# Kernel tuning notes

Hardware: AMD Instinct MI355X
Metric: run time of the kernel (lower is better)

The kernel has to match this reference:

```python
import jax, jax.numpy as jnp
import numpy as np

B, G, C, Hmlp, R = 4, 2048, 384, 1536, 96
NH = 6          # attention heads
V = 6           # number of 2D views (len(out_transform_2d))
NC = 1024       # number of clusters for segment_csr
GX = GY = 32    # grid shape per view
SCALE_FACTOR = 0.5  # args.scale_factor
COEF_PRO = 0.5      # args.coef_pro
EPS_LN = 1e-5
EPS_BN = 1e-5


def _forward(x, center1, norm1_g, norm1_b, qkv_w, proj_w, proj_b, norm2_g, norm2_b,
             fc1_w, fc1_b, fc2_w, fc2_b, ada1_w, ada1_b, ada2_w, ada2_b,
             bn3_g, bn3_b, bn3_m, bn3_v, bn2_g, bn2_b, bn2_m, bn2_v,
             norm3_g, norm3_b, a1_qkv_w, a1_proj_w, a1_proj_b,
             mask, idx_ptr, sorted_cluster_indices, cluster, flat_grid_index,
             grid_shape_x, grid_shape_y):
    B_, G1, C_ = x.shape
    hd = C_ // NH

    def ln(t, g, b):
        mu = t.mean(-1, keepdims=True)
        var = ((t - mu) ** 2).mean(-1, keepdims=True)
        return (t - mu) * jax.lax.rsqrt(var + EPS_LN) * g + b

    def bn_gelu(t, g, b, m, v):  # BatchNorm1d (eval) + GELU
        t = (t - m) * jax.lax.rsqrt(v + EPS_BN) * g + b
        return jax.nn.gelu(t, approximate=False)

    # ---- multi-head self-attention sublayer ----
    h = ln(x, norm1_g, norm1_b)
    qkv = (h @ qkv_w).reshape(B_, G1, 3, NH, hd).transpose(2, 0, 3, 1, 4)
    q, k, v = qkv[0], qkv[1], qkv[2]
    attn = jax.nn.softmax(jnp.einsum('bhqd,bhkd->bhqk', q, k) * hd ** -0.5, axis=-1)
    o = jnp.einsum('bhqk,bhkd->bhqd', attn, v).transpose(0, 2, 1, 3).reshape(B_, G1, C_)
    x = x + o @ proj_w + proj_b

    # ---- MLP + adapter sublayer ----
    h2 = ln(x, norm2_g, norm2_b)
    ffn = jax.nn.gelu(h2 @ fc1_w + fc1_b, approximate=False) @ fc2_w + fc2_b
    a = ffn @ ada1_w + ada1_b
    a = a * jax.nn.sigmoid(1.702 * a)      # QuickGELU
    ada = a @ ada2_w + ada2_b
    x = x + ffn + SCALE_FACTOR * ada

    cls_x = x[:, :1]
    pts = x[:, 1:]
    Gp = G1 - 1
    N = B_ * Gp

    # ---- 3D branch: segment_csr max/mean over clusters, gather back ----
    feat = pts.reshape(N, C_)
    fs = feat[sorted_cluster_indices]
    seg = cluster[sorted_cluster_indices]          # sorted segment ids (CSR order)
    nc = idx_ptr.shape[0] - 1
    cnt = jax.ops.segment_sum(jnp.ones((N,), feat.dtype), seg, nc)
    fsum = jax.ops.segment_sum(fs, seg, nc)
    fmax = jax.ops.segment_max(fs, seg, nc)
    fmax = jnp.where(cnt[:, None] > 0, fmax, 0.0)
    fmean = fsum / jnp.maximum(cnt, 1.0)[:, None]
    x3d = bn_gelu(fmax + fmean, bn3_g, bn3_b, bn3_m, bn3_v)[cluster].reshape(pts.shape)

    # ---- per-view 2D branch: masked attn + scatter_max/mean over grid cells ----
    dim_size = center1.shape[0] * grid_shape_x * grid_shape_y
    nviews = center1.shape[1]
    views = []
    for i in range(nviews):
        fx = pts.reshape(N, C_)
        h3 = ln(fx, norm3_g[i], norm3_b[i]).reshape(B_, Gp, C_)
        qkv1 = (h3 @ a1_qkv_w[i]).reshape(B_, Gp, 3, C_).transpose(2, 0, 1, 3)
        q1, k1, v1 = qkv1[0], qkv1[1], qkv1[2]
        s = jnp.einsum('bqd,bkd->bqk', q1, k1) * C_ ** -0.5
        s = jnp.where(mask[i][None], s, jnp.finfo(s.dtype).min)
        o1 = jnp.einsum('bqk,bkd->bqd', jax.nn.softmax(s, axis=-1), v1) @ a1_proj_w[i] + a1_proj_b[i]
        fx = o1.reshape(N, C_) + fx
        gi = flat_grid_index[i]
        gc = jax.ops.segment_sum(jnp.ones((N,), fx.dtype), gi, dim_size)
        gs = jax.ops.segment_sum(fx, gi, dim_size)
        gm = jax.ops.segment_max(fx, gi, dim_size)
        gm = jnp.where(gc[:, None] > 0, gm, 0.0)
        cell = bn_gelu(gs / jnp.maximum(gc, 1.0)[:, None] + gm,
                       bn2_g[i], bn2_b[i], bn2_m[i], bn2_v[i])
        views.append(cell[gi].reshape(pts.shape))

    # ---- cosine-similarity weighted fusion across views ----
    x_sup = jnp.stack(views, 0)                     # [V,B,G,C]
    dot = jnp.sum(x_sup * x3d[None], -1)
    nrm = jnp.linalg.norm(x_sup, axis=-1) * jnp.linalg.norm(x3d, axis=-1)[None]
    sims = (dot / jnp.maximum(nrm, 1e-8) + 1.0) / 2.0
    sims = sims / sims.sum(0, keepdims=True)
    x_sup_w = jnp.sum(x_sup * sims[..., None], 0)
    pts = pts + COEF_PRO * x_sup_w
    return jnp.concatenate([cls_x, pts], axis=1)


def setup_inputs() -> dict:
    rng = np.random.default_rng(0)
    key = jax.random.key(0)
    N = B * G
    # consistent cluster structure: every cluster non-empty
    cluster = np.concatenate([np.arange(NC), rng.integers(0, NC, N - NC)]).astype(np.int32)
    rng.shuffle(cluster)
    sorted_idx = np.argsort(cluster, kind='stable').astype(np.int32)
    counts = np.bincount(cluster, minlength=NC)
    idx_ptr = np.concatenate([[0], np.cumsum(counts)]).astype(np.int32)
    flat_grid_index = rng.integers(0, B * GX * GY, (V, N)).astype(np.int32)
    mask = (rng.random((V, G, G)) < 0.25) | np.eye(G, dtype=bool)[None]
    ks = jax.random.split(key, 16)
    f32 = jnp.float32
    def w(k, shape, s=0.02):
        return jax.random.normal(k, shape, f32) * s
    return {
        'x': jax.random.normal(ks[0], (B, G + 1, C), f32),
        'center1': jax.random.normal(ks[1], (B, V, G, 3), f32),
        'norm1_g': jnp.ones((C,), f32), 'norm1_b': jnp.zeros((C,), f32),
        'qkv_w': w(ks[2], (C, 3 * C)), 'proj_w': w(ks[3], (C, C)), 'proj_b': jnp.zeros((C,), f32),
        'norm2_g': jnp.ones((C,), f32), 'norm2_b': jnp.zeros((C,), f32),
        'fc1_w': w(ks[4], (C, Hmlp)), 'fc1_b': jnp.zeros((Hmlp,), f32),
        'fc2_w': w(ks[5], (Hmlp, C)), 'fc2_b': jnp.zeros((C,), f32),
        'ada1_w': w(ks[6], (C, R)), 'ada1_b': jnp.zeros((R,), f32),
        'ada2_w': w(ks[7], (R, C)), 'ada2_b': jnp.zeros((C,), f32),
        'bn3_g': jnp.ones((C,), f32), 'bn3_b': jnp.zeros((C,), f32),
        'bn3_m': w(ks[8], (C,), 0.1), 'bn3_v': jnp.ones((C,), f32) + jax.random.uniform(ks[9], (C,), f32) * 0.5,
        'bn2_g': jnp.ones((V, C), f32), 'bn2_b': jnp.zeros((V, C), f32),
        'bn2_m': w(ks[10], (V, C), 0.1), 'bn2_v': jnp.ones((V, C), f32) + jax.random.uniform(ks[11], (V, C), f32) * 0.5,
        'norm3_g': jnp.ones((V, C), f32), 'norm3_b': jnp.zeros((V, C), f32),
        'a1_qkv_w': w(ks[12], (V, C, 3 * C)), 'a1_proj_w': w(ks[13], (V, C, C)), 'a1_proj_b': jnp.zeros((V, C), f32),
        'mask': jnp.asarray(mask),
        'idx_ptr': jnp.asarray(idx_ptr),
        'sorted_cluster_indices': jnp.asarray(sorted_idx),
        'cluster': jnp.asarray(cluster),
        'flat_grid_index': jnp.asarray(flat_grid_index),
        'grid_shape_x': GX,
        'grid_shape_y': GY,
    }


def reference(x, center1, norm1_g, norm1_b, qkv_w, proj_w, proj_b, norm2_g, norm2_b,
              fc1_w, fc1_b, fc2_w, fc2_b, ada1_w, ada1_b, ada2_w, ada2_b,
              bn3_g, bn3_b, bn3_m, bn3_v, bn2_g, bn2_b, bn2_m, bn2_v,
              norm3_g, norm3_b, a1_qkv_w, a1_proj_w, a1_proj_b,
              mask, idx_ptr, sorted_cluster_indices, cluster, flat_grid_index,
              grid_shape_x, grid_shape_y):
    return _forward(x, center1, norm1_g, norm1_b, qkv_w, proj_w, proj_b, norm2_g, norm2_b,
                    fc1_w, fc1_b, fc2_w, fc2_b, ada1_w, ada1_b, ada2_w, ada2_b,
                    bn3_g, bn3_b, bn3_m, bn3_v, bn2_g, bn2_b, bn2_m, bn2_v,
                    norm3_g, norm3_b, a1_qkv_w, a1_proj_w, a1_proj_b,
                    mask, idx_ptr, sorted_cluster_indices, cluster, flat_grid_index,
                    grid_shape_x, grid_shape_y)
```

## Files before the change

### kernel.cpp

```cpp
#include <hip/hip_runtime.h>
#include <math.h>

typedef short bf16x8 __attribute__((ext_vector_type(8)));
typedef float f32x4 __attribute__((ext_vector_type(4)));

#define GLL16(g, l) \
  __builtin_amdgcn_global_load_lds((__attribute__((address_space(1))) const unsigned int*)(g), \
                                   (__attribute__((address_space(3))) unsigned int*)(l), 16, 0, 0)

__device__ __forceinline__ float wsum(float v){
  #pragma unroll
  for (int o=32;o;o>>=1) v += __shfl_xor(v,o);
  return v;
}
__device__ __forceinline__ float geluf(float x){
  return 0.5f*x*(1.0f+erff(x*0.7071067811865475f));
}
__device__ __forceinline__ short fbf(float f){
  unsigned u = __float_as_uint(f);
  unsigned r = (u + 0x7fffu + ((u>>16)&1u)) >> 16;
  return (short)r;
}
__device__ __forceinline__ float bff(short s){
  return __uint_as_float(((unsigned)(unsigned short)s)<<16);
}
__device__ __forceinline__ unsigned fkey(float f){
  unsigned b=__float_as_uint(f);
  return (b&0x80000000u)? ~b : (b|0x80000000u);
}
__device__ __forceinline__ float fdec(unsigned k){
  unsigned b=(k&0x80000000u)? (k&0x7fffffffu) : ~k;
  return __uint_as_float(b);
}

__global__ void mask_bits_kernel(const void* __restrict__ m, unsigned long long* __restrict__ mb,
                                 long long nOut, int mode){
  long long i = (long long)blockIdx.x*256 + threadIdx.x;
  if (i>=nOut) return;
  unsigned long long bits = 0;
  if (mode){
    const unsigned long long* p = (const unsigned long long*)((const unsigned char*)m + i*64);
    #pragma unroll
    for (int k=0;k<8;k++){
      unsigned long long v = p[k];
      #pragma unroll
      for (int b=0;b<8;b++)
        bits |= (unsigned long long)(((v>>(b*8))&0xffull)!=0) << (k*8+b);
    }
  } else {
    const int4* p = (const int4*)((const int*)m + i*64);
    #pragma unroll
    for (int k=0;k<16;k++){
      int4 v = p[k];
      bits |= (unsigned long long)(v.x!=0) << (k*4+0);
      bits |= (unsigned long long)(v.y!=0) << (k*4+1);
      bits |= (unsigned long long)(v.z!=0) << (k*4+2);
      bits |= (unsigned long long)(v.w!=0) << (k*4+3);
    }
  }
  mb[i] = bits;
}

__device__ __forceinline__ float epi(float v, const float* bias, int col, int act){
  if (bias) v += bias[col];
  if (act==1) v = geluf(v);
  else if (act==2) v = v*(1.f/(1.f+__expf(-1.702f*v)));
  return v;
}

#define XBM 128
#define XBN 128
#define XBK 32
__global__ __launch_bounds__(256)
void gemm_bf16_big(const short* __restrict__ A, int lda, long long sA,
                   const short* __restrict__ B, int ldb, long long sB,
                   const float* __restrict__ bias, long long sBias,
                   const float* __restrict__ res, int ldr, long long sR,
                   void* __restrict__ out, int ldo, long long sO, int outbf16,
                   int M, int N, int K, int act, int KS)
{
  __shared__ short As[XBM*XBK];
  __shared__ short Bs[XBN*XBK];
  int zz = blockIdx.z;
  int z = zz / KS, ks = zz - z*KS;
  A += (long long)z*sA; B += (long long)z*sB;
  if (res) res += (long long)z*sR;
  if (bias) bias += (long long)z*sBias;
  float* outF = (float*)out + (long long)z*sO;
  short* outH = (short*)out + (long long)z*sO;

  int tid = threadIdx.x;
  int rowBase = blockIdx.y*XBM;
  int colBase = blockIdx.x*XBN;

  int Kc = ((K + KS*XBK - 1)/(KS*XBK))*XBK;
  int kbeg = ks*Kc;
  int kend = min(K, kbeg+Kc);
  if (kbeg >= kend) return;

  int w = tid>>6;
  int lane = tid&63;
  int lm = lane&15, quad = lane>>4;
  int waveM = w>>1, waveN = w&1;

  int arow0 = min(rowBase + w*32 + lm,      M-1);
  int arow1 = min(rowBase + w*32 + 16 + lm, M-1);
  int brow0 = min(colBase + w*32 + lm,      N-1);
  int brow1 = min(colBase + w*32 + 16 + lm, N-1);
  const short* Ag0 = A + (long long)arow0*lda + quad*8;
  const short* Ag1 = A + (long long)arow1*lda + quad*8;
  const short* Bg0 = B + (long long)brow0*ldb + quad*8;
  const short* Bg1 = B + (long long)brow1*ldb + quad*8;
  short* Al0 = &As[(w*2+0)*512];
  short* Al1 = &As[(w*2+1)*512];
  short* Bl0 = &Bs[(w*2+0)*512];
  short* Bl1 = &Bs[(w*2+1)*512];

  f32x4 acc[4][4] = {};

  for (int k0=kbeg; k0<kend; k0+=XBK){
    GLL16(Ag0 + k0, Al0);
    GLL16(Ag1 + k0, Al1);
    GLL16(Bg0 + k0, Bl0);
    GLL16(Bg1 + k0, Bl1);
    __syncthreads();
    bf16x8 af[4], bfr[4];
    #pragma unroll
    for (int tm=0;tm<4;tm++) af[tm]  = *(bf16x8*)&As[(waveM*4+tm)*512 + quad*128 + lm*8];
    #pragma unroll
    for (int tn=0;tn<4;tn++) bfr[tn] = *(bf16x8*)&Bs[(waveN*4+tn)*512 + quad*128 + lm*8];
    #pragma unroll
    for (int tm=0;tm<4;tm++)
      #pragma unroll
      for (int tn=0;tn<4;tn++)
        acc[tm][tn] = __builtin_amdgcn_mfma_f32_16x16x32_bf16(af[tm], bfr[tn], acc[tm][tn], 0,0,0);
    __syncthreads();
  }

  #pragma unroll
  for (int tm=0;tm<4;tm++){
    #pragma unroll
    for (int tn=0;tn<4;tn++){
      int col = colBase + waveN*64 + tn*16 + lm;
      if (col>=N) continue;
      #pragma unroll
      for (int reg=0;reg<4;reg++){
        int row = rowBase + waveM*64 + tm*16 + quad*4 + reg;
        if (row>=M) continue;
        float v = acc[tm][tn][reg];
        if (KS>1){ atomicAdd(&outF[(long long)row*ldo+col], v); continue; }
        v = epi(v, bias, col, act);
        if (res) v += res[(long long)row*ldr+col];
        if (outbf16) outH[(long long)row*ldo+col] = fbf(v);
        else         outF[(long long)row*ldo+col] = v;
      }
    }
  }
}

__global__ __launch_bounds__(256)
void gemm_bf16_s(const short* __restrict__ A, int lda, long long sA,
                 const short* __restrict__ B, int ldb, long long sB,
                 const float* __restrict__ bias, long long sBias,
                 const float* __restrict__ res, int ldr, long long sR,
                 void* __restrict__ out, int ldo, long long sO, int outbf16,
                 int M, int N, int K, int act, short* __restrict__ out2)
{
  __shared__ short As[64*32];
  __shared__ short Bs[64*32];
  int z = blockIdx.z;
  A += (long long)z*sA; B += (long long)z*sB;
  if (res) res += (long long)z*sR;
  if (bias) bias += (long long)z*sBias;
  float* outF = (float*)out + (long long)z*sO;
  short* outH = (short*)out + (long long)z*sO;

  int tid = threadIdx.x;
  int rowBase = blockIdx.y*64;
  int colBase = blockIdx.x*64;

  int w = tid>>6;
  int lane = tid&63;
  int lm = lane&15, quad = lane>>4;
  int wm = w>>1, wn = w&1;

  int arow = min(rowBase + w*16 + lm, M-1);
  int brow = min(colBase + w*16 + lm, N-1);
  const short* Ag = A + (long long)arow*lda + quad*8;
  const short* Bg = B + (long long)brow*ldb + quad*8;
  short* Al = &As[w*512];
  short* Bl = &Bs[w*512];

  f32x4 acc[2][2] = {};

  for (int k0=0; k0<K; k0+=32){
    GLL16(Ag + k0, Al);
    GLL16(Bg + k0, Bl);
    __syncthreads();
    bf16x8 af[2], bfr[2];
    #pragma unroll
    for (int tm=0;tm<2;tm++) af[tm]  = *(bf16x8*)&As[(wm*2+tm)*512 + quad*128 + lm*8];
    #pragma unroll
    for (int tn=0;tn<2;tn++) bfr[tn] = *(bf16x8*)&Bs[(wn*2+tn)*512 + quad*128 + lm*8];
    #pragma unroll
    for (int tm=0;tm<2;tm++)
      #pragma unroll
      for (int tn=0;tn<2;tn++)
        acc[tm][tn] = __builtin_amdgcn_mfma_f32_16x16x32_bf16(af[tm], bfr[tn], acc[tm][tn], 0,0,0);
    __syncthreads();
  }

  #pragma unroll
  for (int tm=0;tm<2;tm++){
    #pragma unroll
    for (int tn=0;tn<2;tn++){
      int col = colBase + wn*32 + tn*16 + lm;
      if (col>=N) continue;
      #pragma unroll
      for (int reg=0;reg<4;reg++){
        int row = rowBase + wm*32 + tm*16 + quad*4 + reg;
        if (row>=M) continue;
        float v = epi(acc[tm][tn][reg], bias, col, act);
        if (res) v += res[(long long)row*ldr+col];
        if (outbf16==2){
          int bb = row>>11;
          outH[((long long)bb*384 + col)*2176 + (row&2047)] = fbf(v);
        }
        else if (outbf16) outH[(long long)row*ldo+col] = fbf(v);
        else {
          outF[(long long)row*ldo+col] = v;
          if (out2) out2[(long long)row*ldo+col] = fbf(v);
        }
      }
    }
  }
}

__global__ __launch_bounds__(256,2)
void flash_view(const short* __restrict__ QK6, const short* __restrict__ Vt6,
                const unsigned long long* __restrict__ maskbits, short* __restrict__ O6)
{
  __shared__ char lds[58112];
  const float scale = 0.05103103630798288f;
  int id = blockIdx.x;
  int xcd = id & 7;
  int j = id >> 3;
  int vb = xcd*3 + (j>>5);
  int qt = j & 31;
  int v = vb >> 2, b = vb & 3;
  int tid=threadIdx.x, w=tid>>6, lane=tid&63, lm=lane&15, quad=lane>>4;

  const short* Qp = QK6 + ((long long)v*8192 + b*2048 + qt*64)*768;
  const short* Kp = QK6 + ((long long)v*8192 + b*2048)*768 + 384;
  const short* Vp = Vt6 + (long long)(v*4+b)*384*2048;
  const unsigned long long* Mb = maskbits + (long long)v*2048*32 + (long long)qt*64*32;
  short* Op = O6 + ((long long)v*8192 + b*2048 + qt*64)*384;

  short* P = (short*)(lds + 49152);
  float* alphaL = (float*)(lds + 57856);

  bf16x8 af[12];
  #pragma unroll
  for (int c=0;c<12;c++)
    af[c] = *(const bf16x8*)(Qp + (long long)(w*16+lm)*768 + c*32 + quad*8);

  float m_i[4], l_i[4];
  #pragma unroll
  for (int r=0;r<4;r++){ m_i[r]=-3.0e38f; l_i[r]=0.f; }
  f32x4 Oacc[4][6] = {};

  for (int kt=0; kt<32; kt++){
    #pragma unroll
    for (int c=0;c<12;c++)
      GLL16(Kp + (long long)(kt*64 + w*16 + lm)*768 + c*32 + quad*8, (short*)(lds + w*12288 + c*1024));
    __syncthreads();
    unsigned long long mb[4];
    #pragma unroll
    for (int r=0;r<4;r++)
      mb[r] = Mb[(long long)(w*16+quad*4+r)*32 + kt];
    f32x4 S[4];
    #pragma unroll
    for (int i=0;i<4;i++) S[i] = (f32x4){0.f,0.f,0.f,0.f};
    __builtin_amdgcn_s_setprio(1);
    #pragma unroll
    for (int kc=0;kc<12;kc++){
      #pragma unroll
      for (int ct=0;ct<4;ct++){
        bf16x8 bf = *(bf16x8*)(lds + ct*12288 + kc*1024 + quad*256 + lm*16);
        S[ct] = __builtin_amdgcn_mfma_f32_16x16x32_bf16(af[kc], bf, S[ct], 0,0,0);
      }
    }
    __builtin_amdgcn_s_setprio(0);
    #pragma unroll
    for (int r=0;r<4;r++){
      unsigned long long t = mb[r] >> lm;
      S[0][r] = ((unsigned)t      & 1u) ? S[0][r]*scale : -3.0e38f;
      S[1][r] = ((unsigned)(t>>16)& 1u) ? S[1][r]*scale : -3.0e38f;
      S[2][r] = ((unsigned)(t>>32)& 1u) ? S[2][r]*scale : -3.0e38f;
      S[3][r] = ((unsigned)(t>>48)& 1u) ? S[3][r]*scale : -3.0e38f;
    }
    float alpha[4], mnew[4];
    #pragma unroll
    for (int r=0;r<4;r++){
      float rm = S[0][r];
      #pragma unroll
      for (int ct=1;ct<4;ct++) rm = fmaxf(rm, S[ct][r]);
      #pragma unroll
      for (int o=1;o<16;o<<=1) rm = fmaxf(rm, __shfl_xor(rm, o));
      mnew[r] = fmaxf(m_i[r], rm);
      alpha[r] = __expf(m_i[r]-mnew[r]);
      m_i[r] = mnew[r];
    }
    float rs[4] = {0.f,0.f,0.f,0.f};
    #pragma unroll
    for (int ct=0;ct<4;ct++){
      #pragma unroll
      for (int r=0;r<4;r++){
        float sv = S[ct][r];
        float p = (sv > -1.0e37f) ? __expf(sv - mnew[r]) : 0.f;
        rs[r] += p;
        P[(w*16+quad*4+r)*68 + ct*16 + lm] = fbf(p);
      }
    }
    #pragma unroll
    for (int r=0;r<4;r++){
      #pragma unroll
      for (int o=1;o<16;o<<=1) rs[r] += __shfl_xor(rs[r], o);
      l_i[r] = l_i[r]*alpha[r] + rs[r];
    }
    if (lm==0){
      #pragma unroll
      for (int r=0;r<4;r++) alphaL[w*16+quad*4+r] = alpha[r];
    }
    bf16x8 Vreg[6][2];
    #pragma unroll
    for (int jj=0;jj<6;jj++)
      #pragma unroll
      for (int kk=0;kk<2;kk++)
        Vreg[jj][kk] = *(const bf16x8*)(Vp + (long long)((w*6+jj)*16+lm)*2048 + kt*64 + kk*32 + quad*8);
    __syncthreads();
    f32x4 am[4];
    #pragma unroll
    for (int m=0;m<4;m++) am[m] = *(f32x4*)&alphaL[m*16 + quad*4];
    #pragma unroll
    for (int m=0;m<4;m++)
      #pragma unroll
      for (int tn=0;tn<6;tn++)
        Oacc[m][tn] *= am[m];
    __builtin_amdgcn_s_setprio(1);
    #pragma unroll
    for (int kk=0;kk<2;kk++){
      bf16x8 ap[4];
      #pragma unroll
      for (int m=0;m<4;m++) ap[m] = *(bf16x8*)&P[(m*16+lm)*68 + kk*32 + quad*8];
      #pragma unroll
      for (int tn=0;tn<6;tn++){
        #pragma unroll
        for (int m=0;m<4;m++)
          Oacc[m][tn] = __builtin_amdgcn_mfma_f32_16x16x32_bf16(ap[m], Vreg[tn][kk], Oacc[m][tn], 0,0,0);
      }
    }
    __builtin_amdgcn_s_setprio(0);
  }

  __syncthreads();
  if (lm==0){
    #pragma unroll
    for (int r=0;r<4;r++) alphaL[w*16+quad*4+r] = l_i[r];
  }
  __syncthreads();
  f32x4 lv[4];
  #pragma unroll
  for (int m=0;m<4;m++) lv[m] = *(f32x4*)&alphaL[m*16 + quad*4];
  #pragma unroll
  for (int m=0;m<4;m++){
    #pragma unroll
    for (int tn=0;tn<6;tn++){
      #pragma unroll
      for (int reg=0;reg<4;reg++){
        Op[(long long)(m*16+quad*4+reg)*384 + (w*6+tn)*16 + lm] = fbf(Oacc[m][tn][reg] / lv[m][reg]);
      }
    }
  }
}

__global__ __launch_bounds__(256,3)
void flash_inner(const short* __restrict__ QKV, const short* __restrict__ Vt,
                 short* __restrict__ O)
{
  __shared__ char lds[33536];
  int id = blockIdx.x;
  int xcd = id & 7;
  int j = id >> 3;
  int bh = xcd*3 + j/33;
  int qt = j%33;
  int b=bh/6, h=bh-b*6;
  int tid=threadIdx.x, w=tid>>6, lane=tid&63, lm=lane&15, quad=lane>>4;

  const short* Qb = QKV + (long long)b*2049*1152 + h*64;
  const short* Kb = Qb + 384;
  const short* Vtp = Vt + (long long)bh*64*2176;
  short* Op = O + ((long long)b*2049 + qt*64)*384 + h*64;

  short* P = (short*)(lds + 16384);
  float* alphaL = (float*)(lds + 33280);

  int qr = min(qt*64 + w*16 + lm, 2048);
  bf16x8 af[2];
  #pragma unroll
  for (int c=0;c<2;c++)
    af[c] = *(const bf16x8*)(Qb + (long long)qr*1152 + c*32 + quad*8);

  float m_i[4], l_i[4];
  #pragma unroll
  for (int r=0;r<4;r++){ m_i[r]=-3.0e38f; l_i[r]=0.f; }
  f32x4 Oacc[4] = {};

  #pragma unroll
  for (int h2=0;h2<2;h2++){
    int kr0 = min((w*2+h2)*16 + lm, 2048);
    #pragma unroll
    for (int c=0;c<2;c++)
      GLL16(Kb + (long long)kr0*1152 + c*32 + quad*8, (short*)(lds + (w*2+h2)*2048 + c*1024));
  }

  for (int kt=0; kt<17; kt++){
    __syncthreads();
    f32x4 S[8];
    #pragma unroll
    for (int i=0;i<8;i++) S[i] = (f32x4){0.f,0.f,0.f,0.f};
    __builtin_amdgcn_s_setprio(1);
    #pragma unroll
    for (int kc=0;kc<2;kc++){
      #pragma unroll
      for (int ct=0;ct<8;ct++){
        bf16x8 bf = *(bf16x8*)(lds + ct*2048 + kc*1024 + quad*256 + lm*16);
        S[ct] = __builtin_amdgcn_mfma_f32_16x16x32_bf16(af[kc], bf, S[ct], 0,0,0);
      }
    }
    __builtin_amdgcn_s_setprio(0);
    #pragma unroll
    for (int ct=0;ct<8;ct++){
      int scol = kt*128 + ct*16 + lm;
      bool ok = scol <= 2048;
      #pragma unroll
      for (int r=0;r<4;r++) S[ct][r] = ok ? S[ct][r]*0.125f : -3.0e38f;
    }
    float alpha[4], mnew[4];
    #pragma unroll
    for (int r=0;r<4;r++){
      float rm = S[0][r];
      #pragma unroll
      for (int ct=1;ct<8;ct++) rm = fmaxf(rm, S[ct][r]);
      #pragma unroll
      for (int o=1;o<16;o<<=1) rm = fmaxf(rm, __shfl_xor(rm, o));
      mnew[r] = fmaxf(m_i[r], rm);
      alpha[r] = __expf(m_i[r]-mnew[r]);
      m_i[r] = mnew[r];
    }
    float rs[4] = {0.f,0.f,0.f,0.f};
    #pragma unroll
    for (int ct=0;ct<8;ct++){
      #pragma unroll
      for (int r=0;r<4;r++){
        float sv = S[ct][r];
        float p = (sv > -1.0e37f) ? __expf(sv - mnew[r]) : 0.f;
        rs[r] += p;
        P[(w*16+quad*4+r)*132 + ct*16 + lm] = fbf(p);
      }
    }
    #pragma unroll
    for (int r=0;r<4;r++){
      #pragma unroll
      for (int o=1;o<16;o<<=1) rs[r] += __shfl_xor(rs[r], o);
      l_i[r] = l_i[r]*alpha[r] + rs[r];
    }
    if (lm==0){
      #pragma unroll
      for (int r=0;r<4;r++) alphaL[w*16+quad*4+r] = alpha[r];
    }
    bf16x8 Vreg[4];
    #pragma unroll
    for (int kk=0;kk<4;kk++)
      Vreg[kk] = *(const bf16x8*)(Vtp + (long long)(w*16+lm)*2176 + kt*128 + kk*32 + quad*8);
    __syncthreads();
    if (kt < 16){
      #pragma unroll
      for (int h2=0;h2<2;h2++){
        int krn = min((kt+1)*128 + (w*2+h2)*16 + lm, 2048);
        #pragma unroll
        for (int c=0;c<2;c++)
          GLL16(Kb + (long long)krn*1152 + c*32 + quad*8, (short*)(lds + (w*2+h2)*2048 + c*1024));
      }
    }
    f32x4 am[4];
    #pragma unroll
    for (int m=0;m<4;m++) am[m] = *(f32x4*)&alphaL[m*16 + quad*4];
    #pragma unroll
    for (int m=0;m<4;m++) Oacc[m] *= am[m];
    __builtin_amdgcn_s_setprio(1);
    #pragma unroll
    for (int kk=0;kk<4;kk++){
      bf16x8 ap[4];
      #pragma unroll
      for (int m=0;m<4;m++) ap[m] = *(bf16x8*)&P[(m*16+lm)*132 + kk*32 + quad*8];
      #pragma unroll
      for (int m=0;m<4;m++)
        Oacc[m] = __builtin_amdgcn_mfma_f32_16x16x32_bf16(ap[m], Vreg[kk], Oacc[m], 0,0,0);
    }
    __builtin_amdgcn_s_setprio(0);
  }

  __syncthreads();
  if (lm==0){
    #pragma unroll
    for (int r=0;r<4;r++) alphaL[w*16+quad*4+r] = l_i[r];
  }
  __syncthreads();
  f32x4 lv[4];
  #pragma unroll
  for (int m=0;m<4;m++) lv[m] = *(f32x4*)&alphaL[m*16 + quad*4];
  #pragma unroll
  for (int m=0;m<4;m++){
    #pragma unroll
    for (int reg=0;reg<4;reg++){
      int row = qt*64 + m*16 + quad*4 + reg;
      if (row < 2049)
        Op[(long long)(m*16+quad*4+reg)*384 + w*16 + lm] = fbf(Oacc[m][reg] / lv[m][reg]);
    }
  }
}

__global__ __launch_bounds__(128)
void ln_bf16_kernel(const float* __restrict__ in, const float* __restrict__ g,
                    const float* __restrict__ bt, short* __restrict__ out)
{
  long long row = blockIdx.x;
  const float* p = in + row*384;
  int tid = threadIdx.x;
  float v0=p[tid], v1=p[tid+128], v2=p[tid+256];
  float s = v0+v1+v2;
  float ss = v0*v0+v1*v1+v2*v2;
  __shared__ float r1[2], r2[2];
  s = wsum(s); ss = wsum(ss);
  int wid=tid>>6, lane=tid&63;
  if (lane==0){ r1[wid]=s; r2[wid]=ss; }
  __syncthreads();
  float mean=(r1[0]+r1[1])*(1.f/384.f);
  float var =(r2[0]+r2[1])*(1.f/384.f)-mean*mean;
  float rstd=rsqrtf(var+1e-5f);
  short* o = out + row*384;
  o[tid]     = fbf((v0-mean)*rstd*g[tid]+bt[tid]);
  o[tid+128] = fbf((v1-mean)*rstd*g[tid+128]+bt[tid+128]);
  o[tid+256] = fbf((v2-mean)*rstd*g[tid+256]+bt[tid+256]);
}

__global__ __launch_bounds__(128)
void ln6_kernel(const float* __restrict__ in, const float* __restrict__ g6,
                const float* __restrict__ b6, short* __restrict__ out6)
{
  long long row = blockIdx.x;
  const float* p = in + row*384;
  int tid = threadIdx.x;
  float v0=p[tid], v1=p[tid+128], v2=p[tid+256];
  float s = v0+v1+v2;
  float ss = v0*v0+v1*v1+v2*v2;
  __shared__ float r1[2], r2[2];
  s = wsum(s); ss = wsum(ss);
  int wid=tid>>6, lane=tid&63;
  if (lane==0){ r1[wid]=s; r2[wid]=ss; }
  __syncthreads();
  float mean=(r1[0]+r1[1])*(1.f/384.f);
  float var =(r2[0]+r2[1])*(1.f/384.f)-mean*mean;
  float rstd=rsqrtf(var+1e-5f);
  float n0=(v0-mean)*rstd, n1=(v1-mean)*rstd, n2=(v2-mean)*rstd;
  #pragma unroll
  for (int i=0;i<6;i++){
    const float* g = g6 + i*384;
    const float* bt = b6 + i*384;
    short* o = out6 + (long long)i*8192*384 + row*384;
    o[tid]     = fbf(n0*g[tid]+bt[tid]);
    o[tid+128] = fbf(n1*g[tid+128]+bt[tid+128]);
    o[tid+256] = fbf(n2*g[tid+256]+bt[tid+256]);
  }
}

__global__ __launch_bounds__(256)
void tconv_kernel(const float* __restrict__ in, int ldin, long long sIn, long long sIn2, int zmod,
                  int R, int C, short* __restrict__ out, int ldout, long long sOut)
{
  __shared__ float tile[32][33];
  int z = blockIdx.z;
  const float* ip = in + (long long)(z/zmod)*sIn + (long long)(z%zmod)*sIn2;
  short* op = out + (long long)z*sOut;
  int r0 = blockIdx.x*32;
  int c0 = blockIdx.y*32;
  int tx = threadIdx.x&31, ty = threadIdx.x>>5;
  #pragma unroll
  for (int i=0;i<4;i++){
    int r = r0 + ty + i*8, c = c0 + tx;
    tile[ty+i*8][tx] = (r<R && c<C) ? ip[(long long)r*ldin + c] : 0.f;
  }
  __syncthreads();
  #pragma unroll
  for (int i=0;i<4;i++){
    int oc = c0 + ty + i*8;
    int orr = r0 + tx;
    if (oc<C && orr<ldout) op[(long long)oc*ldout + orr] = fbf(tile[tx][ty+i*8]);
  }
}

__global__ __launch_bounds__(256)
void tconv16_kernel(const short* __restrict__ in, int ldin, long long sIn, long long sIn2, int zmod,
                    int R, int C, short* __restrict__ out, int ldout, long long sOut)
{
  __shared__ short tile[32][34];
  int z = blockIdx.z;
  const short* ip = in + (long long)(z/zmod)*sIn + (long long)(z%zmod)*sIn2;
  short* op = out + (long long)z*sOut;
  int r0 = blockIdx.x*32;
  int c0 = blockIdx.y*32;
  int tx = threadIdx.x&31, ty = threadIdx.x>>5;
  #pragma unroll
  for (int i=0;i<4;i++){
    int r = r0 + ty + i*8, c = c0 + tx;
    tile[ty+i*8][tx] = (r<R && c<C) ? ip[(long long)r*ldin + c] : (short)0;
  }
  __syncthreads();
  #pragma unroll
  for (int i=0;i<4;i++){
    int oc = c0 + ty + i*8;
    int orr = r0 + tx;
    if (oc<C && orr<ldout) op[(long long)oc*ldout + orr] = tile[tx][ty+i*8];
  }
}

__global__ void ew_fuse_kernel(const float* __restrict__ x1, const float* __restrict__ ffn,
                               const float* __restrict__ ada,
                               float* __restrict__ ptsb, float* __restrict__ out){
  long long i=(long long)blockIdx.x*256+threadIdx.x;
  if (i >= 8196ll*384) return;
  float v = x1[i] + ffn[i] + 0.5f*ada[i];
  long long row = i/384; int c = (int)(i - row*384);
  long long b = row/2049; long long g = row - b*2049;
  if (g == 0) out[b*2049*384 + c] = v;
  else        ptsb[((b*2048) + (g-1))*384 + c] = v;
}

__global__ __launch_bounds__(128)
void scatter_seg_kernel(const float* __restrict__ feat, const int* __restrict__ seg,
                        float* __restrict__ fsum, unsigned* __restrict__ fmax,
                        float* __restrict__ cnt,
                        long long zFeat, long long zSeg, long long zSum, long long zCnt)
{
  int n = blockIdx.x, z = blockIdx.y;
  feat += (long long)z*zFeat; seg += (long long)z*zSeg;
  fsum += (long long)z*zSum; fmax += (long long)z*zSum; cnt += (long long)z*zCnt;
  int s = seg[n];
  const float* p = feat + (long long)n*384;
  int tid = threadIdx.x;
  #pragma unroll
  for (int k=0;k<3;k++){
    int c = tid + k*128;
    float v = p[c];
    atomicAdd(&fsum[(long long)s*384+c], v);
    atomicMax(&fmax[(long long)s*384+c], fkey(v));
  }
  if (tid==0) atomicAdd(&cnt[s], 1.0f);
}

__global__ __launch_bounds__(128)
void cell_kernel(const float* __restrict__ fsum, const unsigned* __restrict__ fmax,
                 const float* __restrict__ cnt,
                 const float* __restrict__ g, const float* __restrict__ bb,
                 const float* __restrict__ m, const float* __restrict__ v,
                 float* __restrict__ out, long long zSum, long long zCnt, long long zP)
{
  int s = blockIdx.x, z = blockIdx.y;
  fsum += (long long)z*zSum; fmax += (long long)z*zSum; cnt += (long long)z*zCnt;
  g += (long long)z*zP; bb += (long long)z*zP; m += (long long)z*zP; v += (long long)z*zP;
  out += (long long)z*zSum;
  float cn = cnt[s];
  float denom = fmaxf(cn, 1.f);
  int tid = threadIdx.x;
  #pragma unroll
  for (int k=0;k<3;k++){
    int c = tid + k*128;
    float mx = (cn>0.f) ? fdec(fmax[(long long)s*384+c]) : 0.f;
    float t = mx + fsum[(long long)s*384+c]/denom;
    t = (t - m[c])*rsqrtf(v[c]+1e-5f)*g[c] + bb[c];
    out[(long long)s*384+c] = geluf(t);
  }
}

__global__ __launch_bounds__(384)
void combine_kernel(const float* __restrict__ pts, const float* __restrict__ cell3,
                    const int* __restrict__ cluster, const float* __restrict__ cell2,
                    const int* __restrict__ gidx, float* __restrict__ out)
{
  int n = blockIdx.x;
  int tid = threadIdx.x;
  int w = tid>>6, lane = tid&63;
  __shared__ float sdot[6], ssq[6], sn3s;
  __shared__ int soff[6];
  const float* x3 = cell3 + (long long)cluster[n]*384;
  int gi = gidx[(long long)w*8192 + n];
  const float* r = cell2 + ((long long)w*4096 + gi)*384;
  float d=0.f, s2=0.f, q3=0.f;
  #pragma unroll
  for (int k=0;k<6;k++){
    int c = lane + k*64;
    float a = r[c], x = x3[c];
    d += a*x; s2 += a*a; q3 += x*x;
  }
  d = wsum(d); s2 = wsum(s2); q3 = wsum(q3);
  if (lane==0){ sdot[w]=d; ssq[w]=s2; soff[w]=gi; if (w==0) sn3s=q3; }
  __syncthreads();
  float sn3 = sqrtf(sn3s);
  float sims[6]; float ssumv=0.f;
  #pragma unroll
  for (int i=0;i<6;i++){
    float nrm = sqrtf(ssq[i])*sn3;
    float s = (sdot[i]/fmaxf(nrm,1e-8f) + 1.f)*0.5f;
    sims[i]=s; ssumv+=s;
  }
  int c = tid;
  float acc=0.f;
  #pragma unroll
  for (int i=0;i<6;i++){
    const float* rr = cell2 + ((long long)i*4096 + soff[i])*384;
    acc += (sims[i]/ssumv)*rr[c];
  }
  int b = n>>11, gp = n&2047;
  out[((long long)(b*2049 + 1 + gp))*384 + c] = pts[(long long)n*384+c] + 0.5f*acc;
}

static inline void launch_gemm16b(hipStream_t s, const short* A,int lda,long long sA,
  const short* B,int ldb,long long sB, const float* bias, long long sBias,
  const float* res,int ldr,long long sR, void* out,int ldo,long long sO,int outbf16,
  int M,int N,int K,int act,int nz,int KS)
{
  dim3 g((N+XBN-1)/XBN,(M+XBM-1)/XBM,(unsigned)(nz*KS));
  hipLaunchKernelGGL(gemm_bf16_big,g,dim3(256),0,s,
    A,lda,sA,B,ldb,sB,bias,sBias,res,ldr,sR,out,ldo,sO,outbf16,M,N,K,act,KS);
}
static inline void launch_gemm16s(hipStream_t s, const short* A,int lda,long long sA,
  const short* B,int ldb,long long sB, const float* bias, long long sBias,
  const float* res,int ldr,long long sR, void* out,int ldo,long long sO,int outbf16,
  int M,int N,int K,int act,int nz, short* out2=nullptr)
{
  dim3 g((N+63)/64,(M+63)/64,(unsigned)nz);
  hipLaunchKernelGGL(gemm_bf16_s,g,dim3(256),0,s,
    A,lda,sA,B,ldb,sB,bias,sBias,res,ldr,sR,out,ldo,sO,outbf16,M,N,K,act,out2);
}
static inline void launch_tconv(hipStream_t s, const float* in,int ldin,long long sIn,long long sIn2,int zmod,
  int R,int C, short* out,int ldout,long long sOut,int nz)
{
  dim3 g((ldout+31)/32,(C+31)/32,(unsigned)nz);
  hipLaunchKernelGGL(tconv_kernel,g,dim3(256),0,s, in,ldin,sIn,sIn2,zmod,R,C,out,ldout,sOut);
}
static inline void launch_tconv16(hipStream_t s, const short* in,int ldin,long long sIn,long long sIn2,int zmod,
  int R,int C, short* out,int ldout,long long sOut,int nz)
{
  dim3 g((ldout+31)/32,(C+31)/32,(unsigned)nz);
  hipLaunchKernelGGL(tconv16_kernel,g,dim3(256),0,s, in,ldin,sIn,sIn2,zmod,R,C,out,ldout,sOut);
}

extern "C" void kernel_launch(void* const* d_in, const int* in_sizes, int n_in,
                              void* d_out, int out_size, void* d_ws, size_t ws_size,
                              hipStream_t stream)
{
  const float* x       = (const float*)d_in[0];
  const float* norm1_g = (const float*)d_in[2];
  const float* norm1_b = (const float*)d_in[3];
  const float* qkv_w   = (const float*)d_in[4];
  const float* proj_w  = (const float*)d_in[5];
  const float* proj_b  = (const float*)d_in[6];
  const float* norm2_g = (const float*)d_in[7];
  const float* norm2_b = (const float*)d_in[8];
  const float* fc1_w   = (const float*)d_in[9];
  const float* fc1_b   = (const float*)d_in[10];
  const float* fc2_w   = (const float*)d_in[11];
  const float* fc2_b   = (const float*)d_in[12];
  const float* ada1_w  = (const float*)d_in[13];
  const float* ada1_b  = (const float*)d_in[14];
  const float* ada2_w  = (const float*)d_in[15];
  const float* ada2_b  = (const float*)d_in[16];
  const float* bn3_g   = (const float*)d_in[17];
  const float* bn3_b   = (const float*)d_in[18];
  const float* bn3_m   = (const float*)d_in[19];
  const float* bn3_v   = (const float*)d_in[20];
  const float* bn2_g   = (const float*)d_in[21];
  const float* bn2_b   = (const float*)d_in[22];
  const float* bn2_m   = (const float*)d_in[23];
  const float* bn2_v   = (const float*)d_in[24];
  const float* norm3_g = (const float*)d_in[25];
  const float* norm3_b = (const float*)d_in[26];
  const float* a1_qkv_w  = (const float*)d_in[27];
  const float* a1_proj_w = (const float*)d_in[28];
  const float* a1_proj_b = (const float*)d_in[29];
  const void*  maskp     = d_in[30];
  const int*   cluster   = (const int*)d_in[33];
  const int*   fgi       = (const int*)d_in[34];
  float* out = (float*)d_out;

  size_t off = 0;
  char* wsb = (char*)d_ws;
  auto alloc = [&](size_t bytes)->void*{
    void* p = wsb + off;
    off += (bytes + 255) & ~(size_t)255;
    return p;
  };
  short*    bufHh = (short*)alloc(8196ll*384*2);
  float*    ptsb  = (float*)alloc(8192ll*384*4);
  float*    cnt   = (float*)alloc(1024*4);
  float*    fsum  = (float*)alloc(1024ll*384*4);
  unsigned* fmaxe = (unsigned*)alloc(1024ll*384*4);
  float*    cell3 = (float*)alloc(1024ll*384*4);
  unsigned char* maskb = (unsigned char*)alloc(6ll*2048*2048);
  float*    gc6   = (float*)alloc(6ll*4096*4);
  short*    qkvT  = (short*)alloc(1152ll*384*2);
  short*    projT = (short*)alloc(384ll*384*2);
  short*    fc1T  = (short*)alloc(1536ll*384*2);
  short*    fc2T  = (short*)alloc(384ll*1536*2);
  short*    ada1T = (short*)alloc(96ll*384*2);
  short*    ada2T = (short*)alloc(384ll*96*2);
  short*    a1qkvT  = (short*)alloc(6ll*1152*384*2);
  short*    a1projT = (short*)alloc(6ll*384*384*2);
  int*      flag  = (int*)alloc(256);
  char* arena = (char*)alloc(188743680);
  char* A0 = arena;
  char* A1 = arena + 75497472;
  char* A2 = arena + 150994944;
  short* bufQh = (short*)(A0 + 0);
  float* bufO  = (float*)(A0 + 20971520);
  short* bufOh = (short*)(A0 + 35651584);
  short* bufAh = (short*)(A0 + 44040192);
  float* bufX  = (float*)(A0 + 46137344);
  float* bufAda= (float*)(A0 + 0);
  short* Vt_i  = (short*)(A1 + 0);
  short* bufTh = (short*)(A1 + 8388608);
  short* QK6   = (short*)(A0 + 0);
  short* Vt6   = (short*)(A1 + 0);
  short* O6    = (short*)(A2 + 0);
  short* bufHh6= (short*)(A2 + 0);
  float* bufT6 = (float*)(A0 + 0);
  float* gsum6 = (float*)(A1 + 0);
  unsigned* gmaxe6 = (unsigned*)(A1 + 37748736);
  float* cell2 = (float*)(A0 + 0);

  unsigned long long* maskbits = (unsigned long long*)maskb;

  {
    int mode = (in_sizes[30] == 6*2048*2048) ? 1 : 0;
    long long nOut = 6ll*2048*32;
    mask_bits_kernel<<<dim3((unsigned)((nOut+255)/256)),dim3(256),0,stream>>>(maskp, maskbits, nOut, mode);
  }

  launch_tconv(stream, qkv_w, 1152, 0,0,1, 384,1152, qkvT, 384, 0, 1);
  launch_tconv(stream, proj_w, 384, 0,0,1, 384,384,  projT, 384, 0, 1);
  launch_tconv(stream, fc1_w, 1536, 0,0,1, 384,1536, fc1T, 384, 0, 1);
  launch_tconv(stream, fc2_w, 384,  0,0,1, 1536,384, fc2T, 1536, 0, 1);
  launch_tconv(stream, ada1_w, 96,  0,0,1, 384,96,   ada1T, 384, 0, 1);
  launch_tconv(stream, ada2_w, 384, 0,0,1, 96,384,   ada2T, 96, 0, 1);
  launch_tconv(stream, a1_qkv_w, 1152, 384ll*1152,0,1, 384,1152, a1qkvT, 384, 1152ll*384, 6);
  launch_tconv(stream, a1_proj_w, 384, 384ll*384,0,1, 384,384,  a1projT, 384, 384ll*384, 6);

  ln_bf16_kernel<<<8196,128,0,stream>>>(x, norm1_g, norm1_b, bufHh);
  launch_gemm16b(stream, bufHh,384,0, qkvT,384,0, nullptr,0, nullptr,0,0,
                 bufQh,1152,0,1, 8196,1152,384, 0, 1,1);
  launch_tconv16(stream, bufQh + 768, 1152, 2049ll*1152, 64, 6, 2049, 64, Vt_i, 2176, 64ll*2176, 24);
  flash_inner<<<dim3(792),256,0,stream>>>(bufQh, Vt_i, bufOh);
  launch_gemm16s(stream, bufOh,384,0, projT,384,0, proj_b,0, x,384,0,
                 bufX,384,0,0, 8196,384,384, 0, 1);
  ln_bf16_kernel<<<8196,128,0,stream>>>(bufX, norm2_g, norm2_b, bufHh);
  launch_gemm16b(stream, bufHh,384,0, fc1T,384,0, fc1_b,0, nullptr,0,0,
                 bufTh,1536,0,1, 8196,1536,384, 1, 1,1);
  launch_gemm16s(stream, bufTh,1536,0, fc2T,1536,0, fc2_b,0, nullptr,0,0,
                 bufO,384,0,0, 8196,384,1536, 0, 1, bufOh);
  launch_gemm16s(stream, bufOh,384,0, ada1T,384,0, ada1_b,0, nullptr,0,0,
                 bufAh,96,0,1, 8196,96,384, 2, 1);
  launch_gemm16s(stream, bufAh,96,0, ada2T,96,0, ada2_b,0, nullptr,0,0,
                 bufAda,384,0,0, 8196,384,96, 0, 1);
  ew_fuse_kernel<<<dim3((unsigned)((8196ll*384+255)/256)),256,0,stream>>>(bufX, bufO, bufAda, ptsb, out);

  hipMemsetAsync(cnt, 0, 1024*4, stream);
  hipMemsetAsync(fsum, 0, 1024ll*384*4, stream);
  hipMemsetAsync(fmaxe, 0, 1024ll*384*4, stream);
  scatter_seg_kernel<<<dim3(8192,1),128,0,stream>>>(ptsb, cluster, fsum, fmaxe, cnt, 0,0,0,0);
  cell_kernel<<<dim3(1024,1),128,0,stream>>>(fsum, fmaxe, cnt, bn3_g,bn3_b,bn3_m,bn3_v, cell3, 0,0,0);

  ln6_kernel<<<8192,128,0,stream>>>(ptsb, norm3_g, norm3_b, bufHh6);
  launch_gemm16b(stream, bufHh6,384,8192ll*384, a1qkvT,384,1152ll*384,
                 nullptr,0, nullptr,0,0, QK6,768,8192ll*768,1, 8192,768,384, 0, 6,1);
  launch_gemm16s(stream, bufHh6,384,8192ll*384, a1qkvT + 768ll*384,384,1152ll*384,
                 nullptr,0, nullptr,0,0, Vt6,2048,4ll*384*2048,2, 8192,384,384, 0, 6);

  flash_view<<<dim3(768),256,0,stream>>>(QK6, Vt6, maskbits, O6);

  launch_gemm16s(stream, O6,384,8192ll*384, a1projT,384,384ll*384,
                 a1_proj_b,384, ptsb,384,0,
                 bufT6,384,8192ll*384,0, 8192,384,384, 0, 6);
  hipMemsetAsync(gc6, 0, 6ll*4096*4, stream);
  hipMemsetAsync(gsum6, 0, 6ll*4096*384*4, stream);
  hipMemsetAsync(gmaxe6, 0, 6ll*4096*384*4, stream);
  scatter_seg_kernel<<<dim3(8192,6),128,0,stream>>>(bufT6, fgi, gsum6, gmaxe6, gc6,
      8192ll*384, 8192, 4096ll*384, 4096);
  cell_kernel<<<dim3(4096,6),128,0,stream>>>(gsum6, gmaxe6, gc6,
      bn2_g, bn2_b, bn2_m, bn2_v, cell2, 4096ll*384, 4096, 384);

  combine_kernel<<<8192,384,0,stream>>>(ptsb, cell3, cluster, cell2, fgi, out);
}
```

Measured before the change: 1.477 ms.

## Fuse segment scatter reductions into elementwise and projection GEMM epilogues

The cluster scatter (sum, max, count atomics) moves into ew_fuse_kernel, and the per-view grid scatter moves into the epilogue of the a1 projection GEMM through a new outbf16==3 mode. This removes the standalone scatter kernels and the write and re-read of the large fp32 bufT6 intermediate. Separate memsets are merged into larger contiguous ones. The cost is atomics issued straight from the GEMM epilogue in MFMA output order, which may change contention and access patterns. The Vt6 transposed-store stride also changes from 2176 to 2048, which must match what flash_view reads.

```diff
diff --git a/kernel.cpp b/kernel.cpp
--- a/kernel.cpp
+++ b/kernel.cpp
@@ -164,7 +164,9 @@
                  const float* __restrict__ bias, long long sBias,
                  const float* __restrict__ res, int ldr, long long sR,
                  void* __restrict__ out, int ldo, long long sO, int outbf16,
-                 int M, int N, int K, int act, short* __restrict__ out2)
+                 int M, int N, int K, int act, short* __restrict__ out2,
+                 const int* __restrict__ sgi, float* __restrict__ ssum,
+                 unsigned* __restrict__ smax, float* __restrict__ scnt)
 {
   __shared__ short As[64*32];
   __shared__ short Bs[64*32];
@@ -222,9 +224,16 @@
         if (row>=M) continue;
         float v = epi(acc[tm][tn][reg], bias, col, act);
         if (res) v += res[(long long)row*ldr+col];
-        if (outbf16==2){
+        if (outbf16==3){
+          int gi = sgi[(long long)z*8192 + row];
+          long long base = ((long long)z*4096 + gi)*384 + col;
+          atomicAdd(&ssum[base], v);
+          atomicMax(&smax[base], fkey(v));
+          if (col==0) atomicAdd(&scnt[(long long)z*4096 + gi], 1.0f);
+        }
+        else if (outbf16==2){
           int bb = row>>11;
-          outH[((long long)bb*384 + col)*2176 + (row&2047)] = fbf(v);
+          outH[((long long)bb*384 + col)*2048 + (row&2047)] = fbf(v);
         }
         else if (outbf16) outH[(long long)row*ldo+col] = fbf(v);
         else {
@@ -637,36 +646,22 @@
 
 __global__ void ew_fuse_kernel(const float* __restrict__ x1, const float* __restrict__ ffn,
                                const float* __restrict__ ada,
+                               const int* __restrict__ cluster,
+                               float* __restrict__ fsum, unsigned* __restrict__ fmax,
+                               float* __restrict__ cnt,
                                float* __restrict__ ptsb, float* __restrict__ out){
   long long i=(long long)blockIdx.x*256+threadIdx.x;
   if (i >= 8196ll*384) return;
   float v = x1[i] + ffn[i] + 0.5f*ada[i];
   long long row = i/384; int c = (int)(i - row*384);
   long long b = row/2049; long long g = row - b*2049;
-  if (g == 0) out[b*2049*384 + c] = v;
-  else        ptsb[((b*2048) + (g-1))*384 + c] = v;
-}
-
-__global__ __launch_bounds__(128)
-void scatter_seg_kernel(const float* __restrict__ feat, const int* __restrict__ seg,
-                        float* __restrict__ fsum, unsigned* __restrict__ fmax,
-                        float* __restrict__ cnt,
-                        long long zFeat, long long zSeg, long long zSum, long long zCnt)
-{
-  int n = blockIdx.x, z = blockIdx.y;
-  feat += (long long)z*zFeat; seg += (long long)z*zSeg;
-  fsum += (long long)z*zSum; fmax += (long long)z*zSum; cnt += (long long)z*zCnt;
-  int s = seg[n];
-  const float* p = feat + (long long)n*384;
-  int tid = threadIdx.x;
-  #pragma unroll
-  for (int k=0;k<3;k++){
-    int c = tid + k*128;
-    float v = p[c];
-    atomicAdd(&fsum[(long long)s*384+c], v);
-    atomicMax(&fmax[(long long)s*384+c], fkey(v));
-  }
-  if (tid==0) atomicAdd(&cnt[s], 1.0f);
+  if (g == 0){ out[b*2049*384 + c] = v; return; }
+  long long n = b*2048 + (g-1);
+  ptsb[n*384 + c] = v;
+  int s = cluster[n];
+  atomicAdd(&fsum[(long long)s*384 + c], v);
+  atomicMax(&fmax[(long long)s*384 + c], fkey(v));
+  if (c==0) atomicAdd(&cnt[s], 1.0f);
 }
 
 __global__ __launch_bounds__(128)
@@ -747,11 +742,13 @@
 static inline void launch_gemm16s(hipStream_t s, const short* A,int lda,long long sA,
   const short* B,int ldb,long long sB, const float* bias, long long sBias,
   const float* res,int ldr,long long sR, void* out,int ldo,long long sO,int outbf16,
-  int M,int N,int K,int act,int nz, short* out2=nullptr)
+  int M,int N,int K,int act,int nz, short* out2=nullptr,
+  const int* sgi=nullptr, float* ssum=nullptr, unsigned* smax=nullptr, float* scnt=nullptr)
 {
   dim3 g((N+63)/64,(M+63)/64,(unsigned)nz);
   hipLaunchKernelGGL(gemm_bf16_s,g,dim3(256),0,s,
-    A,lda,sA,B,ldb,sB,bias,sBias,res,ldr,sR,out,ldo,sO,outbf16,M,N,K,act,out2);
+    A,lda,sA,B,ldb,sB,bias,sBias,res,ldr,sR,out,ldo,sO,outbf16,M,N,K,act,out2,
+    sgi,ssum,smax,scnt);
 }
 static inline void launch_tconv(hipStream_t s, const float* in,int ldin,long long sIn,long long sIn2,int zmod,
   int R,int C, short* out,int ldout,long long sOut,int nz)
@@ -844,7 +841,6 @@
   short* Vt6   = (short*)(A1 + 0);
   short* O6    = (short*)(A2 + 0);
   short* bufHh6= (short*)(A2 + 0);
-  float* bufT6 = (float*)(A0 + 0);
   float* gsum6 = (float*)(A1 + 0);
   unsigned* gmaxe6 = (unsigned*)(A1 + 37748736);
   float* cell2 = (float*)(A0 + 0);
@@ -882,12 +878,10 @@
                  bufAh,96,0,1, 8196,96,384, 2, 1);
   launch_gemm16s(stream, bufAh,96,0, ada2T,96,0, ada2_b,0, nullptr,0,0,
                  bufAda,384,0,0, 8196,384,96, 0, 1);
-  ew_fuse_kernel<<<dim3((unsigned)((8196ll*384+255)/256)),256,0,stream>>>(bufX, bufO, bufAda, ptsb, out);
-
-  hipMemsetAsync(cnt, 0, 1024*4, stream);
-  hipMemsetAsync(fsum, 0, 1024ll*384*4, stream);
-  hipMemsetAsync(fmaxe, 0, 1024ll*384*4, stream);
-  scatter_seg_kernel<<<dim3(8192,1),128,0,stream>>>(ptsb, cluster, fsum, fmaxe, cnt, 0,0,0,0);
+  hipMemsetAsync(cnt, 0, 4096 + 2*1572864, stream);
+  ew_fuse_kernel<<<dim3((unsigned)((8196ll*384+255)/256)),256,0,stream>>>(
+      bufX, bufO, bufAda, cluster, fsum, fmaxe, cnt, ptsb, out);
+
   cell_kernel<<<dim3(1024,1),128,0,stream>>>(fsum, fmaxe, cnt, bn3_g,bn3_b,bn3_m,bn3_v, cell3, 0,0,0);
 
   ln6_kernel<<<8192,128,0,stream>>>(ptsb, norm3_g, norm3_b, bufHh6);
@@ -898,14 +892,12 @@
 
   flash_view<<<dim3(768),256,0,stream>>>(QK6, Vt6, maskbits, O6);
 
+  hipMemsetAsync(gsum6, 0, 2ll*37748736, stream);
+  hipMemsetAsync(gc6, 0, 6ll*4096*4, stream);
   launch_gemm16s(stream, O6,384,8192ll*384, a1projT,384,384ll*384,
                  a1_proj_b,384, ptsb,384,0,
-                 bufT6,384,8192ll*384,0, 8192,384,384, 0, 6);
-  hipMemsetAsync(gc6, 0, 6ll*4096*4, stream);
-  hipMemsetAsync(gsum6, 0, 6ll*4096*384*4, stream);
-  hipMemsetAsync(gmaxe6, 0, 6ll*4096*384*4, stream);
-  scatter_seg_kernel<<<dim3(8192,6),128,0,stream>>>(bufT6, fgi, gsum6, gmaxe6, gc6,
-      8192ll*384, 8192, 4096ll*384, 4096);
+                 nullptr,384,0,3, 8192,384,384, 0, 6, nullptr,
+                 fgi, gsum6, gmaxe6, gc6);
   cell_kernel<<<dim3(4096,6),128,0,stream>>>(gsum6, gmaxe6, gc6,
       bn2_g, bn2_b, bn2_m, bn2_v, cell2, 4096ll*384, 4096, 384);
 
```

Result: faster. 1.423 ms (-3.6%).
